# Kernel optimization log

Measured on AMD Instinct MI355X. Metric: run time of the kernel, lower is better.

## Reference

```python
import jax, jax.numpy as jnp
import numpy as np

LOG2 = float(np.log(2.0))

def ssp(x):
    # shifted softplus: softplus(x) - log(2)
    return jax.nn.softplus(x) - LOG2

def setup_inputs() -> dict:
    key = jax.random.key(0)
    ks = jax.random.split(key, 12)
    B, N, K, G, Fdim, H, O = 2, 1024, 64, 64, 128, 4, 128
    s = 0.05
    return {
        'x': jax.random.normal(ks[0], (B, N, Fdim), jnp.float32),
        'r_ij': jax.random.uniform(ks[1], (B, N, K), jnp.float32),
        'neighbors': jax.random.randint(ks[2], (B, N, K), 0, N),
        'pairwise_mask': jnp.ones((B, N, K), jnp.float32),
        'f_ij': jax.random.normal(ks[3], (B, N, K, G), jnp.float32),
        'w_in2f': jax.random.normal(ks[4], (H, Fdim, Fdim), jnp.float32) * s,
        'w_att': jax.random.normal(ks[5], (H, 2 * Fdim), jnp.float32) * s,
        'wf1': jax.random.normal(ks[6], (G, Fdim), jnp.float32) * s,
        'bf1': jnp.zeros((Fdim,), jnp.float32),
        'wf2': jax.random.normal(ks[7], (Fdim, Fdim), jnp.float32) * s,
        'bf2': jnp.zeros((Fdim,), jnp.float32),
        'w_out': jax.random.normal(ks[8], (Fdim, O), jnp.float32) * s,
        'b_out': jnp.zeros((O,), jnp.float32),
    }

def reference(x, r_ij, neighbors, pairwise_mask, f_ij,
              w_in2f, w_att, wf1, bf1, wf2, bf2, w_out, b_out):
    B, N, K = neighbors.shape
    H, _, Fdim = w_in2f.shape
    # continuous filter network: MLP on radial features -> [B,N,K,F]
    W = ssp(jnp.einsum('bnkg,gf->bnkf', f_ij, wf1) + bf1)
    W = jnp.einsum('bnkf,fe->bnke', W, wf2) + bf2
    # per-head linear projections: [B,H,N,F]
    y = jnp.einsum('bni,hif->bhnf', x, w_in2f)
    # gather neighbor features along atom axis: [B,H,N,K,F]
    idx = jnp.broadcast_to(neighbors.reshape(B, 1, N * K, 1), (B, H, N * K, Fdim))
    y_nb = jnp.take_along_axis(y, idx, axis=2).reshape(B, H, N, K, Fdim)
    # GAT attention logits via split weight (equiv. to concat + Dense):
    a_c = jnp.einsum('bhnf,hf->bhn', y, w_att[:, :Fdim])       # center part
    a_n = jnp.einsum('bhnkf,hf->bhnk', y_nb, w_att[:, Fdim:])  # neighbor part
    att = a_c[:, :, :, None] + a_n                             # [B,H,N,K]
    alpha = jax.nn.softmax(ssp(att), axis=-1)
    # attention-weighted neighbor features times continuous filters, mean over heads
    out = jnp.einsum('bhnk,bhnkf,bnkf->bnkf', alpha, y_nb, W) / H
    # masked aggregation over the neighbor axis
    agg = jnp.sum(out * pairwise_mask[..., None], axis=2)      # [B,N,F]
    return ssp(jnp.einsum('bnf,fo->bno', agg, w_out) + b_out)
```

## Files before the change

kernel.cpp:

```cpp
#include <hip/hip_runtime.h>

#define NB 2
#define NN 1024
#define NK 64
#define NG 64
#define NF 128
#define NH 4
#define NO 128
#define PITCH 132

typedef unsigned short ushort_t;
typedef __attribute__((ext_vector_type(8))) short short8v;
typedef __attribute__((ext_vector_type(4))) float f32x4;

union FragU { uint4 u4; short8v s8; };

__device__ __forceinline__ float bf2f(ushort_t u) {
    union { unsigned int i; float f; } v; v.i = ((unsigned int)u) << 16; return v.f;
}
__device__ __forceinline__ ushort_t f2bf(float f) {
    unsigned int u = __float_as_uint(f);
    unsigned int r = 0x7fffu + ((u >> 16) & 1u);
    return (ushort_t)((u + r) >> 16);
}
__device__ __forceinline__ float sspf(float x) {
    const float u = __builtin_amdgcn_exp2f(-fabsf(x) * 1.44269504088896341f);
    return fmaxf(x, 0.f) + fmaf(0.69314718055994531f,
                                __builtin_amdgcn_logf(1.f + u),
                                -0.69314718055994531f);
}

__global__ __launch_bounds__(256) void k_projprep(
    const float* __restrict__ x,
    const float* __restrict__ w_in2f,
    const float* __restrict__ w_att,
    const float* __restrict__ wf1, const float* __restrict__ wf2,
    const float* __restrict__ w_out,
    ushort_t* __restrict__ y,
    float* __restrict__ a_c,
    float* __restrict__ a_n,
    ushort_t* __restrict__ wf1f, ushort_t* __restrict__ wf2f,
    float* __restrict__ w_outT)
{
    const int t = threadIdx.x;
    __shared__ float xs[8][NF];
    __shared__ float ys[32][PITCH];

    if (blockIdx.x >= 256) {
        int s = (blockIdx.x - 256) * 256 + t;
        if (s >= 7168) return;
        if (s >= 3072) {
            const int s2 = s - 3072;
            const int o = s2 >> 5, fb = s2 & 31;
            #pragma unroll
            for (int j = 0; j < 4; ++j)
                w_outT[(size_t)o * NF + fb * 4 + j] = w_out[(size_t)(fb * 4 + j) * NO + o];
            return;
        }
        const float* W; ushort_t* out; int loOff;
        if (s < 1024) { W = wf1; out = wf1f; loOff = 8192; }
        else          { s -= 1024; W = wf2; out = wf2f; loOff = 16384; }
        const int fi = s >> 6, lane = s & 63;
        const int ks = fi >> 3, nf = fi & 7;
        const int n = nf * 16 + (lane & 15);
        const int kb = ks * 32 + ((lane >> 4) & 3) * 4;
        #pragma unroll
        for (int j = 0; j < 8; ++j) {
            const int k = kb + (j & 3) + ((j >> 2) << 4);
            const float v = W[(size_t)k * NF + n];
            const ushort_t hb = f2bf(v);
            out[(size_t)(fi * 64 + lane) * 8 + j] = hb;
            out[(size_t)loOff + (fi * 64 + lane) * 8 + j] = f2bf(v - bf2f(hb));
        }
        return;
    }

    const int bn0 = blockIdx.x * 8;
    {
        const float4* src = (const float4*)(x + (size_t)bn0 * NF);
        float4* dst = (float4*)(&xs[0][0]);
        dst[t] = src[t];
    }
    __syncthreads();

    const int hp = t >> 7;
    const int f0 = t & 127;
    const int h0 = hp, h1 = hp + 2;
    const float* w0 = w_in2f + (size_t)h0 * NF * NF + f0;
    const float* w1 = w_in2f + (size_t)h1 * NF * NF + f0;
    float acc0[8], acc1[8];
    #pragma unroll
    for (int n = 0; n < 8; ++n) { acc0[n] = 0.f; acc1[n] = 0.f; }

    for (int i0 = 0; i0 < NF; i0 += 4) {
        float4 xv[8];
        #pragma unroll
        for (int n = 0; n < 8; ++n) xv[n] = *(const float4*)&xs[n][i0];
        #pragma unroll
        for (int ii = 0; ii < 4; ++ii) {
            const float wa = w0[(size_t)(i0 + ii) * NF];
            const float wb = w1[(size_t)(i0 + ii) * NF];
            #pragma unroll
            for (int n = 0; n < 8; ++n) {
                const float xi = (&xv[n].x)[ii];
                acc0[n] = fmaf(xi, wa, acc0[n]);
                acc1[n] = fmaf(xi, wb, acc1[n]);
            }
        }
    }
    #pragma unroll
    for (int n = 0; n < 8; ++n) {
        const int bn = bn0 + n;
        const int b = bn >> 10, nn = bn & (NN - 1);
        y[((size_t)(b * NH + h0) * NN + nn) * NF + f0] = f2bf(acc0[n]);
        y[((size_t)(b * NH + h1) * NN + nn) * NF + f0] = f2bf(acc1[n]);
        ys[n * 4 + h0][f0] = acc0[n];
        ys[n * 4 + h1][f0] = acc1[n];
    }
    __syncthreads();

    {
        const int hn = t >> 3, q = t & 7;
        const int h = hn & 3, n = hn >> 2;
        float pc = 0.f, pn = 0.f;
        #pragma unroll
        for (int j = 0; j < 16; ++j) {
            const int f = q + 8 * j;
            const float yv = ys[n * 4 + h][f];
            pc = fmaf(yv, w_att[h * 2 * NF + f], pc);
            pn = fmaf(yv, w_att[h * 2 * NF + NF + f], pn);
        }
        #pragma unroll
        for (int off = 1; off < 8; off <<= 1) {
            pc += __shfl_xor(pc, off, 8);
            pn += __shfl_xor(pn, off, 8);
        }
        if (q == 0) {
            const int bn = bn0 + n;
            const int b = bn >> 10, nn = bn & (NN - 1);
            a_c[(size_t)(b * NH + h) * NN + nn] = pc;
            a_n[(size_t)(b * NH + h) * NN + nn] = pn;
        }
    }
}

__global__ __launch_bounds__(256, 6) void k_main(
    const int*      __restrict__ neighbors,
    const float*    __restrict__ pmask,
    const float*    __restrict__ f_ij,
    const float*    __restrict__ bf1,
    const float*    __restrict__ bf2v,
    const float*    __restrict__ w_outT,
    const float*    __restrict__ b_out,
    const ushort_t* __restrict__ y,
    const float*    __restrict__ a_c,
    const float*    __restrict__ a_n,
    const ushort_t* __restrict__ wf1f,
    const ushort_t* __restrict__ wf2f,
    float*          __restrict__ outp)
{
    const int bn = blockIdx.x;
    const int b = bn >> 10, n_ = bn & (NN - 1);
    const int t = threadIdx.x;

    __shared__ __align__(16) char smem[22784];
    ushort_t* fijs = (ushort_t*)(smem);
    ushort_t* W1   = (ushort_t*)(smem);
    ushort_t* W2   = (ushort_t*)(smem);
    float*    aggp = (float*)(smem + 16896);
    float*    aggc = (float*)(smem + 20992);
    float*    alpha = (float*)(smem + 21504);
    int*      nbs   = (int*)(smem + 22528);

    const int wave = t >> 6, lane = t & 63;
    const int lrow = lane & 15;
    const int lq   = (lane >> 4) & 3;
    const int wb   = wave * 32;

    {
        const float4* src = (const float4*)(f_ij + (size_t)bn * NK * NG);
        #pragma unroll
        for (int i = 0; i < 4; ++i) {
            const int e4 = i * 256 + t;
            const float4 v = src[e4];
            const int e = e4 * 4;
            const int row = e >> 6, col = e & 63;
            uint2 ph;
            ph.x = (unsigned)f2bf(v.x) | ((unsigned)f2bf(v.y) << 16);
            ph.y = (unsigned)f2bf(v.z) | ((unsigned)f2bf(v.w) << 16);
            *(uint2*)&fijs[row * 68 + col] = ph;
        }
    }
    if (t < NK) nbs[t] = neighbors[(size_t)bn * NK + t];
    __syncthreads();

    const float avc = a_c[(size_t)(b * NH + wave) * NN + n_];
    const float avn = a_n[(size_t)(b * NH + wave) * NN + nbs[lane]];
    const float pmk = pmask[(size_t)bn * NK + lane];

    f32x4 acc[4][2];
    {
        #pragma unroll
        for (int mf = 0; mf < 4; ++mf)
            #pragma unroll
            for (int nf2 = 0; nf2 < 2; ++nf2) acc[mf][nf2] = (f32x4)0.f;

        #pragma unroll
        for (int ks = 0; ks < 2; ++ks) {
            FragU b1h[2], b1l[2];
            #pragma unroll
            for (int nf2 = 0; nf2 < 2; ++nf2) {
                const int fi = ks * 8 + wave * 2 + nf2;
                b1h[nf2].u4 = *((const uint4*)wf1f + fi * 64 + lane);
                b1l[nf2].u4 = *((const uint4*)(wf1f + 8192) + fi * 64 + lane);
            }
            const int cb = ks * 32 + lq * 4;
            #pragma unroll
            for (int mf = 0; mf < 4; ++mf) {
                const int row = mf * 16 + lrow;
                FragU ah;
                {
                    const uint2 p0 = *(const uint2*)&fijs[row * 68 + cb];
                    const uint2 p1 = *(const uint2*)&fijs[row * 68 + cb + 16];
                    uint4 q; q.x = p0.x; q.y = p0.y; q.z = p1.x; q.w = p1.y; ah.u4 = q;
                }
                #pragma unroll
                for (int nf2 = 0; nf2 < 2; ++nf2) {
                    acc[mf][nf2] = __builtin_amdgcn_mfma_f32_16x16x32_bf16(ah.s8, b1h[nf2].s8, acc[mf][nf2], 0, 0, 0);
                    acc[mf][nf2] = __builtin_amdgcn_mfma_f32_16x16x32_bf16(ah.s8, b1l[nf2].s8, acc[mf][nf2], 0, 0, 0);
                }
            }
        }
    }
    __syncthreads();
    {
        const float bia[2] = { bf1[wb + lrow], bf1[wb + 16 + lrow] };
        #pragma unroll
        for (int mf = 0; mf < 4; ++mf)
            #pragma unroll
            for (int nf2 = 0; nf2 < 2; ++nf2) {
                const int col = wb + nf2 * 16 + lrow;
                #pragma unroll
                for (int r = 0; r < 4; ++r) {
                    const int row = mf * 16 + lq * 4 + r;
                    W1[row * 132 + col] = f2bf(sspf(acc[mf][nf2][r] + bia[nf2]));
                }
            }
    }
    __syncthreads();

    {
        #pragma unroll
        for (int mf = 0; mf < 4; ++mf)
            #pragma unroll
            for (int nf2 = 0; nf2 < 2; ++nf2) acc[mf][nf2] = (f32x4)0.f;

        for (int ks = 0; ks < 4; ++ks) {
            FragU b2h[2];
            #pragma unroll
            for (int nf2 = 0; nf2 < 2; ++nf2) {
                const int fi = ks * 8 + wave * 2 + nf2;
                b2h[nf2].u4 = *((const uint4*)wf2f + fi * 64 + lane);
            }
            const int cb = ks * 32 + lq * 4;
            #pragma unroll
            for (int mf = 0; mf < 4; ++mf) {
                const int row = mf * 16 + lrow;
                FragU ah;
                {
                    const uint2 p0 = *(const uint2*)&W1[row * 132 + cb];
                    const uint2 p1 = *(const uint2*)&W1[row * 132 + cb + 16];
                    uint4 q; q.x = p0.x; q.y = p0.y; q.z = p1.x; q.w = p1.y; ah.u4 = q;
                }
                #pragma unroll
                for (int nf2 = 0; nf2 < 2; ++nf2)
                    acc[mf][nf2] = __builtin_amdgcn_mfma_f32_16x16x32_bf16(ah.s8, b2h[nf2].s8, acc[mf][nf2], 0, 0, 0);
            }
        }
    }
    __syncthreads();
    {
        const float bia[2] = { bf2v[wb + lrow], bf2v[wb + 16 + lrow] };
        #pragma unroll
        for (int mf = 0; mf < 4; ++mf)
            #pragma unroll
            for (int nf2 = 0; nf2 < 2; ++nf2) {
                const int col = wb + nf2 * 16 + lrow;
                #pragma unroll
                for (int r = 0; r < 4; ++r) {
                    const int row = mf * 16 + lq * 4 + r;
                    W2[row * 132 + col] = f2bf(acc[mf][nf2][r] + bia[nf2]);
                }
            }
    }

    {
        const float att = sspf(avc + avn);
        float m = att;
        #pragma unroll
        for (int off = 32; off > 0; off >>= 1) m = fmaxf(m, __shfl_xor(m, off, 64));
        const float e = __builtin_amdgcn_exp2f((att - m) * 1.44269504088896341f);
        float s = e;
        #pragma unroll
        for (int off = 32; off > 0; off >>= 1) s += __shfl_xor(s, off, 64);
        alpha[wave * 64 + lane] = (e / s) * pmk;
    }
    __syncthreads();

    {
        const int fq = (t & 31) * 4;
        const int kg = t >> 5;
        float4 accv; accv.x = accv.y = accv.z = accv.w = 0.f;
        const ushort_t* yb = y + (size_t)b * NH * NN * NF;
        #pragma unroll 2
        for (int kk = 0; kk < 8; ++kk) {
            const int k = kg * 8 + kk;
            const int nb = nbs[k];
            const ushort_t* yp = yb + (size_t)nb * NF + fq;
            const uint2 u0 = *(const uint2*)(yp);
            const uint2 u1 = *(const uint2*)(yp + (size_t)NN * NF);
            const uint2 u2 = *(const uint2*)(yp + 2 * (size_t)NN * NF);
            const uint2 u3 = *(const uint2*)(yp + 3 * (size_t)NN * NF);
            const float a0 = alpha[0 * 64 + k], a1 = alpha[1 * 64 + k];
            const float a2 = alpha[2 * 64 + k], a3 = alpha[3 * 64 + k];
            float4 s;
            s.x = fmaf(a3, bf2f((ushort_t)(u3.x & 0xffffu)),
                  fmaf(a2, bf2f((ushort_t)(u2.x & 0xffffu)),
                  fmaf(a1, bf2f((ushort_t)(u1.x & 0xffffu)),
                       a0 * bf2f((ushort_t)(u0.x & 0xffffu)))));
            s.y = fmaf(a3, bf2f((ushort_t)(u3.x >> 16)),
                  fmaf(a2, bf2f((ushort_t)(u2.x >> 16)),
                  fmaf(a1, bf2f((ushort_t)(u1.x >> 16)),
                       a0 * bf2f((ushort_t)(u0.x >> 16)))));
            s.z = fmaf(a3, bf2f((ushort_t)(u3.y & 0xffffu)),
                  fmaf(a2, bf2f((ushort_t)(u2.y & 0xffffu)),
                  fmaf(a1, bf2f((ushort_t)(u1.y & 0xffffu)),
                       a0 * bf2f((ushort_t)(u0.y & 0xffffu)))));
            s.w = fmaf(a3, bf2f((ushort_t)(u3.y >> 16)),
                  fmaf(a2, bf2f((ushort_t)(u2.y >> 16)),
                  fmaf(a1, bf2f((ushort_t)(u1.y >> 16)),
                       a0 * bf2f((ushort_t)(u0.y >> 16)))));
            const uint2 wv = *(const uint2*)&W2[k * 132 + fq];
            accv.x = fmaf(bf2f((ushort_t)(wv.x & 0xffffu)), s.x, accv.x);
            accv.y = fmaf(bf2f((ushort_t)(wv.x >> 16)),     s.y, accv.y);
            accv.z = fmaf(bf2f((ushort_t)(wv.y & 0xffffu)), s.z, accv.z);
            accv.w = fmaf(bf2f((ushort_t)(wv.y >> 16)),     s.w, accv.w);
        }
        *(float4*)&aggp[kg * 128 + fq] = accv;
    }
    __syncthreads();
    if (t < NF) {
        float s = 0.f;
        #pragma unroll
        for (int q = 0; q < 8; ++q) s += aggp[q * 128 + t];
        aggc[t] = s * 0.25f;
    }
    __syncthreads();

    if (t < NO) {
        float z = b_out[t];
        const float4* wr = (const float4*)(w_outT + (size_t)t * NF);
        #pragma unroll 8
        for (int q = 0; q < NF / 4; ++q) {
            const float4 w = wr[q];
            const float4 a = *(const float4*)&aggc[q * 4];
            z = fmaf(a.x, w.x, fmaf(a.y, w.y, fmaf(a.z, w.z, fmaf(a.w, w.w, z))));
        }
        outp[(size_t)bn * NO + t] = sspf(z);
    }
}

extern "C" void kernel_launch(void* const* d_in, const int* in_sizes, int n_in,
                              void* d_out, int out_size, void* d_ws, size_t ws_size,
                              hipStream_t stream) {
    const float* x      = (const float*)d_in[0];
    const int*   nbr    = (const int*)d_in[2];
    const float* pmask  = (const float*)d_in[3];
    const float* f_ij   = (const float*)d_in[4];
    const float* w_in2f = (const float*)d_in[5];
    const float* w_att  = (const float*)d_in[6];
    const float* wf1    = (const float*)d_in[7];
    const float* bf1    = (const float*)d_in[8];
    const float* wf2    = (const float*)d_in[9];
    const float* bf2v   = (const float*)d_in[10];
    const float* w_out  = (const float*)d_in[11];
    const float* b_out  = (const float*)d_in[12];

    ushort_t* yb16  = (ushort_t*)d_ws;
    float*    a_c   = (float*)(yb16 + (size_t)NB * NH * NN * NF);
    float*    a_n   = a_c + (size_t)NB * NH * NN;
    ushort_t* wf1f  = (ushort_t*)(a_n + (size_t)NB * NH * NN);
    ushort_t* wf2f  = wf1f + 16384;
    float*    w_outT = (float*)(wf2f + 32768);

    float* outp = (float*)d_out;

    k_projprep<<<NB * NN / 8 + 28, 256, 0, stream>>>(
        x, w_in2f, w_att, wf1, wf2, w_out, yb16, a_c, a_n, wf1f, wf2f, w_outT);
    k_main<<<NB * NN, 256, 0, stream>>>(nbr, pmask, f_ij, bf1, bf2v,
                                        w_outT, b_out, yb16, a_c, a_n, wf1f, wf2f, outp);
}
```

Baseline: 56.51 us.

## Compute filter MLP transposed in registers, removing shared-memory staging and barriers

The two-layer filter MLP is restructured so each wave owns 16 neighbor rows and computes all 128 features as a transposed MFMA (weights as the A operand, per-row activations as B). This lets the first layer's output be repacked directly into B fragments in registers, removing the f_ij and W1 shared-memory round trips and several __syncthreads. The trade-off is higher register pressure (16 accumulator vectors), which is why the occupancy hint drops from 6 to 5 blocks. Weight fragments are now loaded 8 per k-step per wave, which raises global/L2 weight traffic per block.

```diff
diff --git a/kernel.cpp b/kernel.cpp
--- a/kernel.cpp
+++ b/kernel.cpp
@@ -144,7 +144,7 @@
     }
 }
 
-__global__ __launch_bounds__(256, 6) void k_main(
+__global__ __launch_bounds__(256, 5) void k_main(
     const int*      __restrict__ neighbors,
     const float*    __restrict__ pmask,
     const float*    __restrict__ f_ij,
@@ -164,8 +164,6 @@
     const int t = threadIdx.x;
 
     __shared__ __align__(16) char smem[22784];
-    ushort_t* fijs = (ushort_t*)(smem);
-    ushort_t* W1   = (ushort_t*)(smem);
     ushort_t* W2   = (ushort_t*)(smem);
     float*    aggp = (float*)(smem + 16896);
     float*    aggc = (float*)(smem + 20992);
@@ -175,123 +173,83 @@
     const int wave = t >> 6, lane = t & 63;
     const int lrow = lane & 15;
     const int lq   = (lane >> 4) & 3;
-    const int wb   = wave * 32;
-
-    {
-        const float4* src = (const float4*)(f_ij + (size_t)bn * NK * NG);
-        #pragma unroll
-        for (int i = 0; i < 4; ++i) {
-            const int e4 = i * 256 + t;
-            const float4 v = src[e4];
-            const int e = e4 * 4;
-            const int row = e >> 6, col = e & 63;
-            uint2 ph;
-            ph.x = (unsigned)f2bf(v.x) | ((unsigned)f2bf(v.y) << 16);
-            ph.y = (unsigned)f2bf(v.z) | ((unsigned)f2bf(v.w) << 16);
-            *(uint2*)&fijs[row * 68 + col] = ph;
-        }
-    }
+    const int myk  = wave * 16 + lrow;
+
     if (t < NK) nbs[t] = neighbors[(size_t)bn * NK + t];
-    __syncthreads();
-
-    const float avc = a_c[(size_t)(b * NH + wave) * NN + n_];
-    const float avn = a_n[(size_t)(b * NH + wave) * NN + nbs[lane]];
-    const float pmk = pmask[(size_t)bn * NK + lane];
-
-    f32x4 acc[4][2];
-    {
-        #pragma unroll
-        for (int mf = 0; mf < 4; ++mf)
-            #pragma unroll
-            for (int nf2 = 0; nf2 < 2; ++nf2) acc[mf][nf2] = (f32x4)0.f;
-
+
+    const int   mynb = neighbors[(size_t)bn * NK + lane];
+    const float avc  = a_c[(size_t)(b * NH + wave) * NN + n_];
+    const float avn  = a_n[(size_t)(b * NH + wave) * NN + mynb];
+    const float pmk  = pmask[(size_t)bn * NK + lane];
+
+    FragU fB[2];
+    {
+        const float* frow = f_ij + (size_t)bn * NK * NG + (size_t)myk * NG;
         #pragma unroll
         for (int ks = 0; ks < 2; ++ks) {
-            FragU b1h[2], b1l[2];
-            #pragma unroll
-            for (int nf2 = 0; nf2 < 2; ++nf2) {
-                const int fi = ks * 8 + wave * 2 + nf2;
-                b1h[nf2].u4 = *((const uint4*)wf1f + fi * 64 + lane);
-                b1l[nf2].u4 = *((const uint4*)(wf1f + 8192) + fi * 64 + lane);
-            }
-            const int cb = ks * 32 + lq * 4;
-            #pragma unroll
-            for (int mf = 0; mf < 4; ++mf) {
-                const int row = mf * 16 + lrow;
-                FragU ah;
-                {
-                    const uint2 p0 = *(const uint2*)&fijs[row * 68 + cb];
-                    const uint2 p1 = *(const uint2*)&fijs[row * 68 + cb + 16];
-                    uint4 q; q.x = p0.x; q.y = p0.y; q.z = p1.x; q.w = p1.y; ah.u4 = q;
-                }
-                #pragma unroll
-                for (int nf2 = 0; nf2 < 2; ++nf2) {
-                    acc[mf][nf2] = __builtin_amdgcn_mfma_f32_16x16x32_bf16(ah.s8, b1h[nf2].s8, acc[mf][nf2], 0, 0, 0);
-                    acc[mf][nf2] = __builtin_amdgcn_mfma_f32_16x16x32_bf16(ah.s8, b1l[nf2].s8, acc[mf][nf2], 0, 0, 0);
-                }
-            }
-        }
-    }
-    __syncthreads();
-    {
-        const float bia[2] = { bf1[wb + lrow], bf1[wb + 16 + lrow] };
-        #pragma unroll
-        for (int mf = 0; mf < 4; ++mf)
-            #pragma unroll
-            for (int nf2 = 0; nf2 < 2; ++nf2) {
-                const int col = wb + nf2 * 16 + lrow;
-                #pragma unroll
-                for (int r = 0; r < 4; ++r) {
-                    const int row = mf * 16 + lq * 4 + r;
-                    W1[row * 132 + col] = f2bf(sspf(acc[mf][nf2][r] + bia[nf2]));
-                }
-            }
-    }
-    __syncthreads();
-
-    {
-        #pragma unroll
-        for (int mf = 0; mf < 4; ++mf)
-            #pragma unroll
-            for (int nf2 = 0; nf2 < 2; ++nf2) acc[mf][nf2] = (f32x4)0.f;
-
-        for (int ks = 0; ks < 4; ++ks) {
-            FragU b2h[2];
-            #pragma unroll
-            for (int nf2 = 0; nf2 < 2; ++nf2) {
-                const int fi = ks * 8 + wave * 2 + nf2;
-                b2h[nf2].u4 = *((const uint4*)wf2f + fi * 64 + lane);
-            }
-            const int cb = ks * 32 + lq * 4;
-            #pragma unroll
-            for (int mf = 0; mf < 4; ++mf) {
-                const int row = mf * 16 + lrow;
-                FragU ah;
-                {
-                    const uint2 p0 = *(const uint2*)&W1[row * 132 + cb];
-                    const uint2 p1 = *(const uint2*)&W1[row * 132 + cb + 16];
-                    uint4 q; q.x = p0.x; q.y = p0.y; q.z = p1.x; q.w = p1.y; ah.u4 = q;
-                }
-                #pragma unroll
-                for (int nf2 = 0; nf2 < 2; ++nf2)
-                    acc[mf][nf2] = __builtin_amdgcn_mfma_f32_16x16x32_bf16(ah.s8, b2h[nf2].s8, acc[mf][nf2], 0, 0, 0);
-            }
-        }
-    }
-    __syncthreads();
-    {
-        const float bia[2] = { bf2v[wb + lrow], bf2v[wb + 16 + lrow] };
-        #pragma unroll
-        for (int mf = 0; mf < 4; ++mf)
-            #pragma unroll
-            for (int nf2 = 0; nf2 < 2; ++nf2) {
-                const int col = wb + nf2 * 16 + lrow;
-                #pragma unroll
-                for (int r = 0; r < 4; ++r) {
-                    const int row = mf * 16 + lq * 4 + r;
-                    W2[row * 132 + col] = f2bf(acc[mf][nf2][r] + bia[nf2]);
-                }
-            }
+            const float4 p0 = *(const float4*)(frow + ks * 32 + lq * 4);
+            const float4 p1 = *(const float4*)(frow + ks * 32 + lq * 4 + 16);
+            uint4 q;
+            q.x = (unsigned)f2bf(p0.x) | ((unsigned)f2bf(p0.y) << 16);
+            q.y = (unsigned)f2bf(p0.z) | ((unsigned)f2bf(p0.w) << 16);
+            q.z = (unsigned)f2bf(p1.x) | ((unsigned)f2bf(p1.y) << 16);
+            q.w = (unsigned)f2bf(p1.z) | ((unsigned)f2bf(p1.w) << 16);
+            fB[ks].u4 = q;
+        }
+    }
+
+    f32x4 cW1[8];
+    #pragma unroll
+    for (int it = 0; it < 8; ++it) cW1[it] = (f32x4)0.f;
+    #pragma unroll
+    for (int ks = 0; ks < 2; ++ks) {
+        #pragma unroll
+        for (int it = 0; it < 8; ++it) {
+            FragU ah, al;
+            ah.u4 = *((const uint4*)wf1f + (ks * 8 + it) * 64 + lane);
+            al.u4 = *((const uint4*)(wf1f + 8192) + (ks * 8 + it) * 64 + lane);
+            cW1[it] = __builtin_amdgcn_mfma_f32_16x16x32_bf16(ah.s8, fB[ks].s8, cW1[it], 0, 0, 0);
+            cW1[it] = __builtin_amdgcn_mfma_f32_16x16x32_bf16(al.s8, fB[ks].s8, cW1[it], 0, 0, 0);
+        }
+    }
+
+    FragU w1B[4];
+    #pragma unroll
+    for (int ks = 0; ks < 4; ++ks) {
+        unsigned e0[4], e1[4];
+        #pragma unroll
+        for (int j = 0; j < 4; ++j) {
+            e0[j] = (unsigned)f2bf(sspf(cW1[2 * ks][j]     + bf1[(2 * ks) * 16     + lq * 4 + j]));
+            e1[j] = (unsigned)f2bf(sspf(cW1[2 * ks + 1][j] + bf1[(2 * ks + 1) * 16 + lq * 4 + j]));
+        }
+        uint4 q;
+        q.x = e0[0] | (e0[1] << 16);
+        q.y = e0[2] | (e0[3] << 16);
+        q.z = e1[0] | (e1[1] << 16);
+        q.w = e1[2] | (e1[3] << 16);
+        w1B[ks].u4 = q;
+    }
+
+    f32x4 cW2[8];
+    #pragma unroll
+    for (int ft = 0; ft < 8; ++ft) cW2[ft] = (f32x4)0.f;
+    #pragma unroll
+    for (int ks = 0; ks < 4; ++ks) {
+        #pragma unroll
+        for (int ft = 0; ft < 8; ++ft) {
+            FragU a2;
+            a2.u4 = *((const uint4*)wf2f + (ks * 8 + ft) * 64 + lane);
+            cW2[ft] = __builtin_amdgcn_mfma_f32_16x16x32_bf16(a2.s8, w1B[ks].s8, cW2[ft], 0, 0, 0);
+        }
+    }
+
+    #pragma unroll
+    for (int ft = 0; ft < 8; ++ft) {
+        const int f0 = ft * 16 + lq * 4;
+        uint2 pk;
+        pk.x = (unsigned)f2bf(cW2[ft][0] + bf2v[f0])     | ((unsigned)f2bf(cW2[ft][1] + bf2v[f0 + 1]) << 16);
+        pk.y = (unsigned)f2bf(cW2[ft][2] + bf2v[f0 + 2]) | ((unsigned)f2bf(cW2[ft][3] + bf2v[f0 + 3]) << 16);
+        *(uint2*)&W2[myk * 132 + f0] = pk;
     }
 
     {
```

Measured after the change: 67.16 us. 1.19x slower.
